# Performance work log

Hardware: AMD Instinct MI355X
Metric: run time of the kernel (lower is better)

## Reference

```python
import jax, jax.numpy as jnp
import numpy as np
from jax import lax

P = 10  # patch_size


def _conv(x, w, b, pad):
    y = lax.conv_general_dilated(x, w, (1, 1), [(pad, pad), (pad, pad)],
                                 dimension_numbers=('NCHW', 'OIHW', 'NCHW'))
    return y + b[None, :, None, None]


def setup_inputs() -> dict:
    key = jax.random.key(0)
    ks = jax.random.split(key, 9)
    B, Cin, H, W = 8, 3, 320, 320
    classes = 2
    p2 = P * P
    s = 0.05
    return {
        'x': jax.random.normal(ks[0], (B, Cin, H, W), jnp.float32),
        'w_conv1': jax.random.normal(ks[1], (64, Cin, 7, 7), jnp.float32) * s,
        'b_conv1': jax.random.normal(ks[2], (64,), jnp.float32) * s,
        'w_conv2': jax.random.normal(ks[3], (classes, 64, 3, 3), jnp.float32) * s,
        'b_conv2': jax.random.normal(ks[4], (classes,), jnp.float32) * s,
        'w_fm': jax.random.normal(ks[5], (classes, Cin, 1, 1), jnp.float32) * s,
        'b_fm': jax.random.normal(ks[6], (classes,), jnp.float32) * s,
        'w_lin1': jax.random.normal(ks[7], (2 * p2, p2), jnp.float32) * s,  # torch Linear [out,in]
        'w_lin2': jax.random.normal(ks[8], (p2, 2 * p2), jnp.float32) * s,
    }


def reference(x, w_conv1, b_conv1, w_conv2, b_conv2, w_fm, b_fm, w_lin1, w_lin2):
    p = P
    ini = _conv(_conv(x, w_conv1, b_conv1, 3), w_conv2, b_conv2, 1)  # [B,classes,H,W]
    fea = _conv(x, w_fm, b_fm, 0) / 4.0                              # [B,classes,H,W]
    B, C, H, W = ini.shape
    L = (H // p) * (W // p)

    def unfold(t):  # non-overlapping patches: [B,C,H,W] -> [B,C,L,p*p]
        t = t.reshape(B, C, H // p, p, W // p, p)
        return t.transpose(0, 1, 2, 4, 3, 5).reshape(B, C, L, p * p)

    def trans(t):  # Linear(p2->2p2) -> Linear(2p2->p2) -> ReLU, per patch
        h = jnp.einsum('bclp,qp->bclq', t, w_lin1)
        return jax.nn.relu(jnp.einsum('bclq,pq->bclp', h, w_lin2))

    ui = trans(unfold(ini))   # [B,C,L,p2]
    uf = trans(unfold(fea))   # [B,C,L,p2]
    att = jnp.einsum('bclp,bcmp->bclm', ui, uf) / (p * p)  # [B,C,L,L]
    return att
```

## Files before the change

kernel.cpp:

```cpp
#include <hip/hip_runtime.h>

#define WS_M      0
#define WS_K      10000
#define WS_BETA   12646
#define WS_W9     12664
#define WS_BT     13150
#define WS_UIT    (16384 + 1638400)
#define WS_UFT    (16384 + 2*1638400)

typedef short bf16x8 __attribute__((ext_vector_type(8)));
typedef float f32x4  __attribute__((ext_vector_type(4)));

__device__ inline ushort f2bf(float f) {
    unsigned u = __float_as_uint(f);
    unsigned r = (u + 0x7fffu + ((u >> 16) & 1u)) >> 16;
    return (ushort)r;
}

__global__ __launch_bounds__(256) void k_prep(const float* __restrict__ wl1,
                                              const float* __restrict__ wl2,
                                              const float* __restrict__ wc1,
                                              const float* __restrict__ bc1,
                                              const float* __restrict__ wc2,
                                              const float* __restrict__ bc2,
                                              float* __restrict__ ws) {
    int blk = blockIdx.x;
    int t = threadIdx.x;
    if (blk < 40) {
        int idx = blk * 256 + t;
        if (idx < 10000) {
            int p = idx / 100, r = idx % 100;
            float s = 0.f;
            for (int q = 0; q < 200; ++q)
                s += wl2[p * 200 + q] * wl1[q * 100 + r];
            ws[WS_M + r * 100 + p] = s;
        }
        return;
    }
    __shared__ float swc1[9408];
    __shared__ float swc2[1152];
    __shared__ float sBeta[18];
    for (int i = t; i < 9408; i += 256) swc1[i] = wc1[i];
    for (int i = t; i < 1152; i += 256) swc2[i] = wc2[i];
    __syncthreads();
    if (blk < 43) {
        int base = (blk - 40) * 882;
        for (int ii = t; ii < 882; ii += 256) {
            int idx = base + ii;
            int v = idx % 7; int t1 = idx / 7;
            int u = t1 % 7;  int t2 = t1 / 7;
            int ci = t2 % 3; int t3 = t2 / 3;
            int b = t3 % 3;  int t4 = t3 / 3;
            int a = t4 % 3;  int c = t4 / 3;
            float s = 0.f;
            for (int c64 = 0; c64 < 64; ++c64)
                s += swc2[((c * 64 + c64) * 3 + a) * 3 + b] *
                     swc1[((c64 * 3 + ci) * 7 + u) * 7 + v];
            ws[WS_K + idx] = s;
        }
        if (blk == 40) {
            if (t < 18) {
                int b = t % 3; int a = (t / 3) % 3; int c = t / 9;
                float s = 0.f;
                for (int c64 = 0; c64 < 64; ++c64)
                    s += swc2[((c * 64 + c64) * 3 + a) * 3 + b] * bc1[c64];
                sBeta[t] = s; ws[WS_BETA + t] = s;
            }
            __syncthreads();
            if (t < 2) {
                float s = bc2[t];
                for (int j2 = 0; j2 < 9; ++j2) s += sBeta[t * 9 + j2];
                ws[WS_BT + t] = s;
            }
        }
    } else {
        int idx = (blk - 43) * 243 + t;
        if (t < 243) {
            int dx = idx % 9; int t1 = idx / 9;
            int dy = t1 % 9;  int t2 = t1 / 9;
            int ci = t2 % 3;  int c = t2 / 3;
            float s = 0.f;
            for (int a = 0; a < 3; ++a) {
                int u = dy - a; if (u < 0 || u > 6) continue;
                for (int b = 0; b < 3; ++b) {
                    int v = dx - b; if (v < 0 || v > 6) continue;
                    for (int c64 = 0; c64 < 64; ++c64)
                        s += swc2[((c * 64 + c64) * 3 + a) * 3 + b] *
                             swc1[((c64 * 3 + ci) * 7 + u) * 7 + v];
                }
            }
            ws[WS_W9 + idx] = s;
        }
    }
}

__global__ __launch_bounds__(256, 8) void k_fuse(const float* __restrict__ x,
                                                 const float* __restrict__ wfm,
                                                 const float* __restrict__ bfm,
                                                 const float* __restrict__ ws,
                                                 ushort* __restrict__ uiL,
                                                 ushort* __restrict__ ufL) {
    union alignas(16) SMemU {
        float  sx[3][28][36];
        ushort sOut[2][4][128];
    };
    __shared__ SMemU smu;
    __shared__ float sP[2][100][8];
    const int bx = blockIdx.x, by = blockIdx.y, b = blockIdx.z;
    const int t = threadIdx.x;
    const float* Mt   = ws + WS_M;
    const float* Kw   = ws + WS_K;
    const float* Beta = ws + WS_BETA;
    const float* W9   = ws + WS_W9;
    const float* Bt   = ws + WS_BT;
    const int gh0 = by * 20, gw0 = bx * 20;

    for (int idx = t; idx < 3 * 28 * 28; idx += 256) {
        int ci = idx / 784; int rem = idx - ci * 784;
        int rr = rem / 28, cc = rem - rr * 28;
        int gh = gh0 - 4 + rr, gw = gw0 - 4 + cc;
        float v = 0.f;
        if ((unsigned)gh < 320u && (unsigned)gw < 320u)
            v = x[(b * 3 + ci) * 102400 + gh * 320 + gw];
        smu.sx[ci][rr][cc] = v;
    }
    __syncthreads();

    const int lh = t / 10, lw0 = (t % 10) * 2;
    if (t < 200) {
        float acc0[2], acc1[2];
        float bt0 = Bt[0], bt1 = Bt[1];
        acc0[0] = bt0; acc0[1] = bt0; acc1[0] = bt1; acc1[1] = bt1;
        #pragma unroll
        for (int ci = 0; ci < 3; ++ci) {
            #pragma unroll
            for (int dy = 0; dy < 9; ++dy) {
                const float* xr = &smu.sx[ci][lh + dy][lw0];
                float2 y0 = *(const float2*)(xr);
                float2 y1 = *(const float2*)(xr + 2);
                float2 y2 = *(const float2*)(xr + 4);
                float2 y3 = *(const float2*)(xr + 6);
                float2 y4 = *(const float2*)(xr + 8);
                float xv[10] = {y0.x, y0.y, y1.x, y1.y, y2.x,
                                y2.y, y3.x, y3.y, y4.x, y4.y};
                #pragma unroll
                for (int dx = 0; dx < 9; ++dx) {
                    float w0t = W9[ci * 81 + dy * 9 + dx];
                    float w1t = W9[243 + ci * 81 + dy * 9 + dx];
                    acc0[0] += w0t * xv[dx];
                    acc0[1] += w0t * xv[dx + 1];
                    acc1[0] += w1t * xv[dx];
                    acc1[1] += w1t * xv[dx + 1];
                }
            }
        }
        #pragma unroll
        for (int j = 0; j < 2; ++j) {
            int lw = lw0 + j;
            int li = (lh / 10) * 2 + lw / 10;
            int r  = (lh % 10) * 10 + lw % 10;
            sP[0][r][li] = acc0[j];
            sP[1][r][li] = acc1[j];
        }
    }
    __syncthreads();

    bool edgeblk = (by == 0) | (by == 15) | (bx == 0) | (bx == 15);
    if (edgeblk) {
        for (int e = t; e < 400; e += 256) {
            int elh = e / 20, elw = e % 20;
            int h = gh0 + elh, w = gw0 + elw;
            if (h == 0 || h == 319 || w == 0 || w == 319) {
                float c0 = 0.f, c1 = 0.f;
                for (int a = 0; a < 3; ++a) {
                    int hh = h + a - 1;
                    for (int bb = 0; bb < 3; ++bb) {
                        int wwp = w + bb - 1;
                        bool invalid = ((unsigned)hh >= 320u) | ((unsigned)wwp >= 320u);
                        if (invalid) {
                            c0 += Beta[a * 3 + bb];
                            c1 += Beta[9 + a * 3 + bb];
                            for (int ci = 0; ci < 3; ++ci) {
                                const float* Kc = Kw + ((a * 3 + bb) * 3 + ci) * 49;
                                #pragma unroll
                                for (int u = 0; u < 7; ++u) {
                                    #pragma unroll
                                    for (int v = 0; v < 7; ++v) {
                                        float xv = smu.sx[ci][elh + a + u][elw + bb + v];
                                        c0 += Kc[u * 7 + v] * xv;
                                        c1 += Kc[1323 + u * 7 + v] * xv;
                                    }
                                }
                            }
                        }
                    }
                }
                int li = (elh / 10) * 2 + elw / 10;
                int r  = (elh % 10) * 10 + elw % 10;
                sP[0][r][li] -= c0;
                sP[1][r][li] -= c1;
            }
        }
    }
    __syncthreads();

    auto trans_compute = [&]() {
        if (t < 200) {
            int plane = (t >= 100) ? 1 : 0;
            int p = t - plane * 100;
            float acc[4] = {0.f, 0.f, 0.f, 0.f};
            #pragma unroll 4
            for (int r = 0; r < 100; ++r) {
                float m = Mt[r * 100 + p];
                f32x4 s = *(const f32x4*)&sP[plane][r][0];
                #pragma unroll
                for (int k = 0; k < 4; ++k) acc[k] += m * s[k];
            }
            #pragma unroll
            for (int k = 0; k < 4; ++k)
                smu.sOut[plane][k][p] = f2bf(fmaxf(acc[k], 0.f));
        } else {
            int task = t - 200;
            int plane = task / 28; int rem = task % 28;
            int k = rem / 7, q = rem % 7;
            *(uint2*)&smu.sOut[plane][k][100 + q * 4] = make_uint2(0u, 0u);
        }
    };
    auto writeout = [&](ushort* outL) {
        if (t < 128) {
            int row = t >> 4;
            int plane = row >> 2, k = row & 3;
            int lane16 = t & 15;
            int bc = b * 2 + plane;
            int l = (by * 2 + (k >> 1)) * 32 + bx * 2 + (k & 1);
            uint4 v = *(const uint4*)&smu.sOut[plane][k][lane16 * 8];
            *(uint4*)&outL[((size_t)bc * 1024 + l) * 128 + lane16 * 8] = v;
        }
    };

    trans_compute();
    __syncthreads();
    writeout(uiL);
    if (t < 200) {
        float wf00 = wfm[0], wf01 = wfm[1], wf02 = wfm[2];
        float wf10 = wfm[3], wf11 = wfm[4], wf12 = wfm[5];
        float bf0 = bfm[0], bf1 = bfm[1];
        int gh = gh0 + lh, gwb = gw0 + lw0;
        size_t base = (size_t)b * 3 * 102400 + gh * 320 + gwb;
        float2 c0v = *(const float2*)&x[base];
        float2 c1v = *(const float2*)&x[base + 102400];
        float2 c2v = *(const float2*)&x[base + 204800];
        float s0[2] = {c0v.x, c0v.y};
        float s1[2] = {c1v.x, c1v.y};
        float s2[2] = {c2v.x, c2v.y};
        #pragma unroll
        for (int j = 0; j < 2; ++j) {
            float v0 = (bf0 + s0[j] * wf00 + s1[j] * wf01 + s2[j] * wf02) * 0.25f;
            float v1 = (bf1 + s0[j] * wf10 + s1[j] * wf11 + s2[j] * wf12) * 0.25f;
            int lw = lw0 + j;
            int li = (lh / 10) * 2 + lw / 10;
            int r  = (lh % 10) * 10 + lw % 10;
            sP[0][r][li] = v0;
            sP[1][r][li] = v1;
        }
    }
    __syncthreads();

    trans_compute();
    __syncthreads();
    writeout(ufL);
}

__global__ __launch_bounds__(256) void k_att(const ushort* __restrict__ ui,
                                             const ushort* __restrict__ uf,
                                             float* __restrict__ out) {
    int bc   = blockIdx.z;
    int row0 = blockIdx.y * 64, col0 = blockIdx.x * 128;
    int wave = threadIdx.x >> 6, lane = threadIdx.x & 63;
    int r0 = row0 + (wave >> 1) * 32;
    int c0 = col0 + (wave & 1) * 64;
    int m = lane & 15, quad = lane >> 4;
    const ushort* ub = ui + (size_t)bc * 1024 * 128;
    const ushort* vb = uf + (size_t)bc * 1024 * 128;
    f32x4 acc[2][4];
    #pragma unroll
    for (int i = 0; i < 2; ++i)
        #pragma unroll
        for (int j = 0; j < 4; ++j)
            acc[i][j] = (f32x4){0.f, 0.f, 0.f, 0.f};
    #pragma unroll
    for (int k0 = 0; k0 < 128; k0 += 32) {
        bf16x8 af[2], bfr[4];
        #pragma unroll
        for (int i = 0; i < 2; ++i)
            af[i] = *(const bf16x8*)&ub[(size_t)(r0 + i * 16 + m) * 128 + k0 + quad * 8];
        #pragma unroll
        for (int j = 0; j < 4; ++j)
            bfr[j] = *(const bf16x8*)&vb[(size_t)(c0 + j * 16 + m) * 128 + k0 + quad * 8];
        #pragma unroll
        for (int i = 0; i < 2; ++i)
            #pragma unroll
            for (int j = 0; j < 4; ++j)
                acc[i][j] = __builtin_amdgcn_mfma_f32_16x16x32_bf16(af[i], bfr[j], acc[i][j], 0, 0, 0);
    }
    #pragma unroll
    for (int i = 0; i < 2; ++i) {
        #pragma unroll
        for (int r = 0; r < 4; ++r) {
            int row = r0 + i * 16 + quad * 4 + r;
            float* o = out + ((size_t)bc * 1024 + row) * 1024;
            #pragma unroll
            for (int j = 0; j < 4; ++j)
                o[c0 + j * 16 + m] = acc[i][j][r] * 0.01f;
        }
    }
}

extern "C" void kernel_launch(void* const* d_in, const int* in_sizes, int n_in,
                              void* d_out, int out_size, void* d_ws, size_t ws_size,
                              hipStream_t stream) {
    const float* x       = (const float*)d_in[0];
    const float* w_conv1 = (const float*)d_in[1];
    const float* b_conv1 = (const float*)d_in[2];
    const float* w_conv2 = (const float*)d_in[3];
    const float* b_conv2 = (const float*)d_in[4];
    const float* w_fm    = (const float*)d_in[5];
    const float* b_fm    = (const float*)d_in[6];
    const float* w_lin1  = (const float*)d_in[7];
    const float* w_lin2  = (const float*)d_in[8];
    float* out = (float*)d_out;
    float* ws  = (float*)d_ws;
    ushort* uiL = (ushort*)(ws + WS_UIT);
    ushort* ufL = (ushort*)(ws + WS_UFT);

    k_prep<<<45, 256, 0, stream>>>(w_lin1, w_lin2, w_conv1, b_conv1, w_conv2, b_conv2, ws);
    k_fuse<<<dim3(16, 16, 8), 256, 0, stream>>>(x, w_fm, b_fm, ws, uiL, ufL);
    k_att<<<dim3(8, 16, 16), 256, 0, stream>>>(uiL, ufL, out);
}
```

Before: 204.8 us.

## Merge ini and fea patch transforms into one pass with vectorized tile loads

Computes the fea 1x1 projection from the already-staged shared-memory input tile instead of reloading x from global memory. Both patch matrices are then transformed by the shared linear map in a single loop that reads each Mt element once for two accumulator sets, and they are written out together, which removes two barriers and a second pass over Mt. Interior blocks load the halo tile with float4 instead of scalar loads. The cost is double-sized sP/sOut shared buffers and more registers, so the occupancy hint is lowered from 8 to 6.

```diff
diff --git a/kernel.cpp b/kernel.cpp
--- a/kernel.cpp
+++ b/kernel.cpp
@@ -94,7 +94,7 @@
     }
 }
 
-__global__ __launch_bounds__(256, 8) void k_fuse(const float* __restrict__ x,
+__global__ __launch_bounds__(256, 6) void k_fuse(const float* __restrict__ x,
                                                  const float* __restrict__ wfm,
                                                  const float* __restrict__ bfm,
                                                  const float* __restrict__ ws,
@@ -102,10 +102,10 @@
                                                  ushort* __restrict__ ufL) {
     union alignas(16) SMemU {
         float  sx[3][28][36];
-        ushort sOut[2][4][128];
+        ushort sOut[2][2][4][128];
     };
     __shared__ SMemU smu;
-    __shared__ float sP[2][100][8];
+    __shared__ float sP[2][2][100][8];
     const int bx = blockIdx.x, by = blockIdx.y, b = blockIdx.z;
     const int t = threadIdx.x;
     const float* Mt   = ws + WS_M;
@@ -114,15 +114,26 @@
     const float* W9   = ws + WS_W9;
     const float* Bt   = ws + WS_BT;
     const int gh0 = by * 20, gw0 = bx * 20;
-
-    for (int idx = t; idx < 3 * 28 * 28; idx += 256) {
-        int ci = idx / 784; int rem = idx - ci * 784;
-        int rr = rem / 28, cc = rem - rr * 28;
-        int gh = gh0 - 4 + rr, gw = gw0 - 4 + cc;
-        float v = 0.f;
-        if ((unsigned)gh < 320u && (unsigned)gw < 320u)
-            v = x[(b * 3 + ci) * 102400 + gh * 320 + gw];
-        smu.sx[ci][rr][cc] = v;
+    bool edgeblk = (by == 0) | (by == 15) | (bx == 0) | (bx == 15);
+
+    if (!edgeblk) {
+        for (int i = t; i < 588; i += 256) {
+            int ci = i / 196; int rem = i - ci * 196;
+            int rr = rem / 7, c4 = rem - rr * 7;
+            float4 v = *(const float4*)&x[(b * 3 + ci) * 102400 +
+                                          (gh0 - 4 + rr) * 320 + (gw0 - 4) + c4 * 4];
+            *(float4*)&smu.sx[ci][rr][c4 * 4] = v;
+        }
+    } else {
+        for (int idx = t; idx < 3 * 28 * 28; idx += 256) {
+            int ci = idx / 784; int rem = idx - ci * 784;
+            int rr = rem / 28, cc = rem - rr * 28;
+            int gh = gh0 - 4 + rr, gw = gw0 - 4 + cc;
+            float v = 0.f;
+            if ((unsigned)gh < 320u && (unsigned)gw < 320u)
+                v = x[(b * 3 + ci) * 102400 + gh * 320 + gw];
+            smu.sx[ci][rr][cc] = v;
+        }
     }
     __syncthreads();
 
@@ -154,18 +165,25 @@
                 }
             }
         }
+        float wf00 = wfm[0], wf01 = wfm[1], wf02 = wfm[2];
+        float wf10 = wfm[3], wf11 = wfm[4], wf12 = wfm[5];
+        float bf0 = bfm[0], bf1 = bfm[1];
         #pragma unroll
         for (int j = 0; j < 2; ++j) {
             int lw = lw0 + j;
             int li = (lh / 10) * 2 + lw / 10;
             int r  = (lh % 10) * 10 + lw % 10;
-            sP[0][r][li] = acc0[j];
-            sP[1][r][li] = acc1[j];
-        }
-    }
-    __syncthreads();
-
-    bool edgeblk = (by == 0) | (by == 15) | (bx == 0) | (bx == 15);
+            sP[0][0][r][li] = acc0[j];
+            sP[0][1][r][li] = acc1[j];
+            float s0 = smu.sx[0][4 + lh][4 + lw];
+            float s1 = smu.sx[1][4 + lh][4 + lw];
+            float s2 = smu.sx[2][4 + lh][4 + lw];
+            sP[1][0][r][li] = (bf0 + s0 * wf00 + s1 * wf01 + s2 * wf02) * 0.25f;
+            sP[1][1][r][li] = (bf1 + s0 * wf10 + s1 * wf11 + s2 * wf12) * 0.25f;
+        }
+    }
+    __syncthreads();
+
     if (edgeblk) {
         for (int e = t; e < 400; e += 256) {
             int elh = e / 20, elw = e % 20;
@@ -197,78 +215,57 @@
                 }
                 int li = (elh / 10) * 2 + elw / 10;
                 int r  = (elh % 10) * 10 + elw % 10;
-                sP[0][r][li] -= c0;
-                sP[1][r][li] -= c1;
-            }
-        }
-    }
-    __syncthreads();
-
-    auto trans_compute = [&]() {
-        if (t < 200) {
-            int plane = (t >= 100) ? 1 : 0;
-            int p = t - plane * 100;
-            float acc[4] = {0.f, 0.f, 0.f, 0.f};
-            #pragma unroll 4
-            for (int r = 0; r < 100; ++r) {
-                float m = Mt[r * 100 + p];
-                f32x4 s = *(const f32x4*)&sP[plane][r][0];
-                #pragma unroll
-                for (int k = 0; k < 4; ++k) acc[k] += m * s[k];
-            }
+                sP[0][0][r][li] -= c0;
+                sP[0][1][r][li] -= c1;
+            }
+        }
+    }
+    __syncthreads();
+
+    if (t < 200) {
+        int plane = (t >= 100) ? 1 : 0;
+        int p = t - plane * 100;
+        float ai[4] = {0.f, 0.f, 0.f, 0.f};
+        float af[4] = {0.f, 0.f, 0.f, 0.f};
+        #pragma unroll 4
+        for (int r = 0; r < 100; ++r) {
+            float m = Mt[r * 100 + p];
+            f32x4 si = *(const f32x4*)&sP[0][plane][r][0];
+            f32x4 sf = *(const f32x4*)&sP[1][plane][r][0];
             #pragma unroll
-            for (int k = 0; k < 4; ++k)
-                smu.sOut[plane][k][p] = f2bf(fmaxf(acc[k], 0.f));
-        } else {
-            int task = t - 200;
-            int plane = task / 28; int rem = task % 28;
-            int k = rem / 7, q = rem % 7;
-            *(uint2*)&smu.sOut[plane][k][100 + q * 4] = make_uint2(0u, 0u);
-        }
-    };
-    auto writeout = [&](ushort* outL) {
-        if (t < 128) {
-            int row = t >> 4;
-            int plane = row >> 2, k = row & 3;
-            int lane16 = t & 15;
-            int bc = b * 2 + plane;
-            int l = (by * 2 + (k >> 1)) * 32 + bx * 2 + (k & 1);
-            uint4 v = *(const uint4*)&smu.sOut[plane][k][lane16 * 8];
-            *(uint4*)&outL[((size_t)bc * 1024 + l) * 128 + lane16 * 8] = v;
-        }
-    };
-
-    trans_compute();
-    __syncthreads();
-    writeout(uiL);
-    if (t < 200) {
-        float wf00 = wfm[0], wf01 = wfm[1], wf02 = wfm[2];
-        float wf10 = wfm[3], wf11 = wfm[4], wf12 = wfm[5];
-        float bf0 = bfm[0], bf1 = bfm[1];
-        int gh = gh0 + lh, gwb = gw0 + lw0;
-        size_t base = (size_t)b * 3 * 102400 + gh * 320 + gwb;
-        float2 c0v = *(const float2*)&x[base];
-        float2 c1v = *(const float2*)&x[base + 102400];
-        float2 c2v = *(const float2*)&x[base + 204800];
-        float s0[2] = {c0v.x, c0v.y};
-        float s1[2] = {c1v.x, c1v.y};
-        float s2[2] = {c2v.x, c2v.y};
-        #pragma unroll
-        for (int j = 0; j < 2; ++j) {
-            float v0 = (bf0 + s0[j] * wf00 + s1[j] * wf01 + s2[j] * wf02) * 0.25f;
-            float v1 = (bf1 + s0[j] * wf10 + s1[j] * wf11 + s2[j] * wf12) * 0.25f;
-            int lw = lw0 + j;
-            int li = (lh / 10) * 2 + lw / 10;
-            int r  = (lh % 10) * 10 + lw % 10;
-            sP[0][r][li] = v0;
-            sP[1][r][li] = v1;
-        }
-    }
-    __syncthreads();
-
-    trans_compute();
-    __syncthreads();
-    writeout(ufL);
+            for (int k = 0; k < 4; ++k) {
+                ai[k] += m * si[k];
+                af[k] += m * sf[k];
+            }
+        }
+        #pragma unroll
+        for (int k = 0; k < 4; ++k) {
+            smu.sOut[0][plane][k][p] = f2bf(fmaxf(ai[k], 0.f));
+            smu.sOut[1][plane][k][p] = f2bf(fmaxf(af[k], 0.f));
+        }
+    } else {
+        #pragma unroll
+        for (int pass = 0; pass < 2; ++pass) {
+            int task = (t - 200) + pass * 56;
+            int mat = task / 56; int rem = task % 56;
+            int plane = rem / 28; int rem2 = rem % 28;
+            int k = rem2 / 7, q = rem2 % 7;
+            *(uint2*)&smu.sOut[mat][plane][k][100 + q * 4] = make_uint2(0u, 0u);
+        }
+    }
+    __syncthreads();
+
+    {
+        int mat = t >> 7;
+        int row = (t >> 4) & 7;
+        int plane = row >> 2, k = row & 3;
+        int lane16 = t & 15;
+        int bc = b * 2 + plane;
+        int l = (by * 2 + (k >> 1)) * 32 + bx * 2 + (k & 1);
+        ushort* dst = mat ? ufL : uiL;
+        uint4 v = *(const uint4*)&smu.sOut[mat][plane][k][lane16 * 8];
+        *(uint4*)&dst[((size_t)bc * 1024 + l) * 128 + lane16 * 8] = v;
+    }
 }
 
 __global__ __launch_bounds__(256) void k_att(const ushort* __restrict__ ui,
```

Result: faster. 198.3 us (-3.2%).
